# Performance work log

Measured on AMD Instinct MI355X. Metric: run time of the kernel, lower is better.

The kernel has to match this reference:

```python
import jax, jax.numpy as jnp
import numpy as np

D_IN = 200   # 4 * d_embeddings
H = 64       # hidden_size

def setup_inputs() -> dict:
    key = jax.random.key(0)
    ks = jax.random.split(key, 7)
    B, T = 4096, 128
    s_ih = 1.0 / np.sqrt(H)
    x = jax.random.normal(ks[0], (B, T, D_IN), dtype=jnp.float32)
    W_ih = jax.random.uniform(ks[1], (H, D_IN), minval=-s_ih, maxval=s_ih, dtype=jnp.float32)
    W_hh = jax.random.uniform(ks[2], (H, H), minval=-s_ih, maxval=s_ih, dtype=jnp.float32)
    b_ih = jax.random.uniform(ks[3], (H,), minval=-s_ih, maxval=s_ih, dtype=jnp.float32)
    b_hh = jax.random.uniform(ks[4], (H,), minval=-s_ih, maxval=s_ih, dtype=jnp.float32)
    W_out = jax.random.uniform(ks[5], (1, H), minval=-s_ih, maxval=s_ih, dtype=jnp.float32)
    b_out = jax.random.uniform(ks[6], (1,), minval=-s_ih, maxval=s_ih, dtype=jnp.float32)
    return {"x": x, "W_ih": W_ih, "W_hh": W_hh, "b_ih": b_ih, "b_hh": b_hh,
            "W_out": W_out, "b_out": b_out}

def reference(x, W_ih, W_hh, b_ih, b_hh, W_out, b_out):
    B = x.shape[0]
    # precompute input projection for all timesteps: [B, T, H]
    xp = jnp.einsum('btd,hd->bth', x, W_ih) + b_ih + b_hh
    def step(h, xt):
        h = jnp.tanh(xt + h @ W_hh.T)
        return h, None
    h0 = jnp.zeros((B, H), dtype=x.dtype)
    h_last, _ = jax.lax.scan(step, h0, jnp.swapaxes(xp, 0, 1))  # scan over time
    return jax.nn.sigmoid(h_last @ W_out.T + b_out)  # [B, 1]
```

## Files before the change

### kernel.cpp

```cpp
#include <hip/hip_runtime.h>
#include <hip/hip_bf16.h>


#define TSEQ 128
#define DIN  200
#define HID  64
#define TC   4
#define NCH  (TSEQ/TC)

typedef short bf16x8 __attribute__((ext_vector_type(8)));
typedef float f32x4  __attribute__((ext_vector_type(4)));

__device__ __forceinline__ short f2bf(float f) {
  __hip_bfloat16 h = __float2bfloat16(f);
  return __builtin_bit_cast(short, h);
}
__device__ __forceinline__ bf16x8 cvt8(f32x4 a, f32x4 b) {
  bf16x8 r;
#pragma unroll
  for (int i = 0; i < 4; ++i) { r[i] = f2bf(a[i]); r[4 + i] = f2bf(b[i]); }
  return r;
}
__device__ __forceinline__ float tanh_fast(float x) {
  float e = exp2f(x * 2.885390081777927f);
  float r = __builtin_amdgcn_rcpf(1.f + e);
  return __builtin_fmaf(-2.f, r, 1.f);
}

__global__ __launch_bounds__(256, 1) void rnn_fused(
    const float* __restrict__ x,   const float* __restrict__ Wih,
    const float* __restrict__ Whh, const float* __restrict__ bih,
    const float* __restrict__ bhh, const float* __restrict__ Wout,
    const float* __restrict__ bout, float* __restrict__ out)
{
  __shared__ float          xps[4][TC][HID][4];
  __shared__ unsigned short hb [4][4][HID];

  const int tid  = threadIdx.x;
  const int w    = tid >> 6;
  const int lane = tid & 63;
  const int m    = lane & 15;
  const int g    = lane >> 4;
  const int bw   = blockIdx.x * 16 + w * 4;

  const float* xrow = x + ((size_t)(bw + (m >> 2)) * TSEQ + (m & 3)) * DIN;

  f32x4 pA[7][2], pB[7][2];
  auto LOADC = [&](f32x4 (&P)[7][2], int c) {
    const float* p = xrow + (size_t)c * (TC * DIN);
#pragma unroll
    for (int ks = 0; ks < 7; ++ks) {
      const int d = ks * 32 + g * 8;
      if (d + 8 <= DIN) {
        P[ks][0] = *reinterpret_cast<const f32x4*>(p + d);
        P[ks][1] = *reinterpret_cast<const f32x4*>(p + d + 4);
      } else {
        P[ks][0] = (f32x4)0.f; P[ks][1] = (f32x4)0.f;
      }
    }
  };
  LOADC(pA, 0);
  LOADC(pB, 1);

  bf16x8 wihf[4][7];
#pragma unroll
  for (int nt = 0; nt < 4; ++nt) {
    const float* wr = Wih + (size_t)(nt * 16 + m) * DIN;
#pragma unroll
    for (int ks = 0; ks < 7; ++ks) {
      const int d = ks * 32 + g * 8;
      if (d + 8 <= DIN)
        wihf[nt][ks] = cvt8(*reinterpret_cast<const f32x4*>(wr + d),
                            *reinterpret_cast<const f32x4*>(wr + d + 4));
      else
        wihf[nt][ks] = (bf16x8)0;
    }
  }
  bf16x8 whhf[4][2];
#pragma unroll
  for (int nt = 0; nt < 4; ++nt)
#pragma unroll
    for (int hf = 0; hf < 2; ++hf) {
      const float* wr = Whh + (size_t)(nt * 16 + m) * HID + hf * 32 + g * 8;
      whhf[nt][hf] = cvt8(*reinterpret_cast<const f32x4*>(wr),
                          *reinterpret_cast<const f32x4*>(wr + 4));
    }
  float biasv[4];
#pragma unroll
  for (int nt = 0; nt < 4; ++nt) biasv[nt] = bih[nt * 16 + m] + bhh[nt * 16 + m];
  const float woutv = Wout[g * 16 + m];
  const float bout0 = bout[0];

  reinterpret_cast<unsigned int*>(&hb[w][0][0])[lane]      = 0u;
  reinterpret_cast<unsigned int*>(&hb[w][0][0])[lane + 64] = 0u;

  float vf[4];

  auto BODY = [&](f32x4 (&P)[7][2], int c) {
    bf16x8 afr[7];
#pragma unroll
    for (int ks = 0; ks < 7; ++ks) afr[ks] = cvt8(P[ks][0], P[ks][1]);
    if (c + 2 < NCH) LOADC(P, c + 2);

    f32x4 acc[4];
#pragma unroll
    for (int nt = 0; nt < 4; ++nt) acc[nt] = (f32x4)(biasv[nt]);
#pragma unroll
    for (int ks = 0; ks < 7; ++ks)
#pragma unroll
      for (int nt = 0; nt < 4; ++nt)
        acc[nt] = __builtin_amdgcn_mfma_f32_16x16x32_bf16(afr[ks], wihf[nt][ks], acc[nt], 0, 0, 0);

#pragma unroll
    for (int nt = 0; nt < 4; ++nt)
#pragma unroll
      for (int rr = 0; rr < 4; ++rr)
        xps[w][rr][nt * 16 + m][g] = acc[nt][rr];

#pragma unroll
    for (int tl = 0; tl < TC; ++tl) {
      f32x4 racc[4];
#pragma unroll
      for (int nt = 0; nt < 4; ++nt)
        racc[nt] = *reinterpret_cast<const f32x4*>(&xps[w][tl][nt * 16 + m][0]);
      bf16x8 ha0 = *reinterpret_cast<const bf16x8*>(&hb[w][m & 3][g * 8]);
      bf16x8 ha1 = *reinterpret_cast<const bf16x8*>(&hb[w][m & 3][32 + g * 8]);
#pragma unroll
      for (int nt = 0; nt < 4; ++nt) {
        racc[nt] = __builtin_amdgcn_mfma_f32_16x16x32_bf16(ha0, whhf[nt][0], racc[nt], 0, 0, 0);
        racc[nt] = __builtin_amdgcn_mfma_f32_16x16x32_bf16(ha1, whhf[nt][1], racc[nt], 0, 0, 0);
      }
#pragma unroll
      for (int r = 0; r < 4; ++r) {
        float v = (g == 0) ? racc[0][r] : (g == 1) ? racc[1][r]
                 : (g == 2) ? racc[2][r] : racc[3][r];
        v = tanh_fast(v);
        vf[r] = v;
        hb[w][r][g * 16 + m] = (unsigned short)f2bf(v);
      }
    }
  };

  for (int c = 0; c < NCH; c += 2) { BODY(pA, c); BODY(pB, c + 1); }

  f32x4 s;
#pragma unroll
  for (int r = 0; r < 4; ++r) s[r] = vf[r] * woutv;
#pragma unroll
  for (int mask = 1; mask < 64; mask <<= 1) {
#pragma unroll
    for (int r = 0; r < 4; ++r) s[r] += __shfl_xor(s[r], mask, 64);
  }
  if (lane == 0) {
    f32x4 o;
#pragma unroll
    for (int r = 0; r < 4; ++r) {
      const float z = s[r] + bout0;
      o[r] = __builtin_amdgcn_rcpf(1.f + exp2f(-z * 1.4426950408889634f));
    }
    *reinterpret_cast<f32x4*>(out + bw) = o;
  }
}

extern "C" void kernel_launch(void* const* d_in, const int* in_sizes, int n_in,
                              void* d_out, int out_size, void* d_ws, size_t ws_size,
                              hipStream_t stream) {
  const float* x    = (const float*)d_in[0];
  const float* Wih  = (const float*)d_in[1];
  const float* Whh  = (const float*)d_in[2];
  const float* bih  = (const float*)d_in[3];
  const float* bhh  = (const float*)d_in[4];
  const float* Wout = (const float*)d_in[5];
  const float* bout = (const float*)d_in[6];
  float* out = (float*)d_out;

  const int B = in_sizes[0] / (TSEQ * DIN);
  rnn_fused<<<dim3(B / 16), dim3(256), 0, stream>>>(x, Wih, Whh, bih, bhh, Wout, bout, out);
}
```

Before: 106.3 us.

## Split recurrence into two independent MFMA chains and software-pipeline the projection

The recurrent step now splits the 4 sequences per wave into two groups of 2 rows, each with its own MFMA accumulator chain (ra/rb), interleaved so the two dependency chains can hide each other's MFMA latency. The input projection for the next chunk is double-buffered in shared memory and issued ahead of the recurrent steps of the current chunk, with duplicated writes so each MFMA A-operand row holds the right sequence. This targets the serial latency of the recurrence. In exchange it uses more shared memory and duplicates stores, and only half of each MFMA's output rows carry useful work.

```diff
diff --git a/kernel.cpp b/kernel.cpp
--- a/kernel.cpp
+++ b/kernel.cpp
@@ -33,8 +33,8 @@
     const float* __restrict__ bhh, const float* __restrict__ Wout,
     const float* __restrict__ bout, float* __restrict__ out)
 {
-  __shared__ float          xps[4][TC][HID][4];
-  __shared__ unsigned short hb [4][4][HID];
+  __shared__ float          xps[2][4][2][TC][HID][4];
+  __shared__ unsigned short hb [4][2][2][HID];
 
   const int tid  = threadIdx.x;
   const int w    = tid >> 6;
@@ -47,10 +47,10 @@
 
   f32x4 pA[7][2], pB[7][2];
   auto LOADC = [&](f32x4 (&P)[7][2], int c) {
-    const float* p = xrow + (size_t)c * (TC * DIN);
 #pragma unroll
     for (int ks = 0; ks < 7; ++ks) {
       const int d = ks * 32 + g * 8;
+      const float* p = xrow + (size_t)c * (TC * DIN);
       if (d + 8 <= DIN) {
         P[ks][0] = *reinterpret_cast<const f32x4*>(p + d);
         P[ks][1] = *reinterpret_cast<const f32x4*>(p + d + 4);
@@ -59,8 +59,7 @@
       }
     }
   };
-  LOADC(pA, 0);
-  LOADC(pB, 1);
+  LOADC(pA, 0); LOADC(pB, 1);
 
   bf16x8 wihf[4][7];
 #pragma unroll
@@ -91,17 +90,13 @@
   const float woutv = Wout[g * 16 + m];
   const float bout0 = bout[0];
 
-  reinterpret_cast<unsigned int*>(&hb[w][0][0])[lane]      = 0u;
-  reinterpret_cast<unsigned int*>(&hb[w][0][0])[lane + 64] = 0u;
-
-  float vf[4];
-
-  auto BODY = [&](f32x4 (&P)[7][2], int c) {
+  reinterpret_cast<unsigned int*>(&hb[w][0][0][0])[lane]      = 0u;
+  reinterpret_cast<unsigned int*>(&hb[w][0][0][0])[lane + 64] = 0u;
+
+  auto PROJ = [&](f32x4 (&P)[7][2], float (*xq)[TC][HID][4]) {
     bf16x8 afr[7];
 #pragma unroll
     for (int ks = 0; ks < 7; ++ks) afr[ks] = cvt8(P[ks][0], P[ks][1]);
-    if (c + 2 < NCH) LOADC(P, c + 2);
-
     f32x4 acc[4];
 #pragma unroll
     for (int nt = 0; nt < 4; ++nt) acc[nt] = (f32x4)(biasv[nt]);
@@ -110,42 +105,69 @@
 #pragma unroll
       for (int nt = 0; nt < 4; ++nt)
         acc[nt] = __builtin_amdgcn_mfma_f32_16x16x32_bf16(afr[ks], wihf[nt][ks], acc[nt], 0, 0, 0);
-
 #pragma unroll
     for (int nt = 0; nt < 4; ++nt)
 #pragma unroll
-      for (int rr = 0; rr < 4; ++rr)
-        xps[w][rr][nt * 16 + m][g] = acc[nt][rr];
-
+      for (int rr = 0; rr < 4; ++rr) {
+        float v = acc[nt][rr];
+        float* bp = &xq[g >> 1][rr][nt * 16 + m][0];
+        bp[g & 1] = v; bp[(g & 1) + 2] = v;
+      }
+  };
+
+  float vf0 = 0.f, vf1 = 0.f, vf2 = 0.f, vf3 = 0.f;
+
+  auto STEPS = [&](float (*xq)[TC][HID][4]) {
 #pragma unroll
     for (int tl = 0; tl < TC; ++tl) {
-      f32x4 racc[4];
-#pragma unroll
-      for (int nt = 0; nt < 4; ++nt)
-        racc[nt] = *reinterpret_cast<const f32x4*>(&xps[w][tl][nt * 16 + m][0]);
-      bf16x8 ha0 = *reinterpret_cast<const bf16x8*>(&hb[w][m & 3][g * 8]);
-      bf16x8 ha1 = *reinterpret_cast<const bf16x8*>(&hb[w][m & 3][32 + g * 8]);
+      f32x4 ra[4], rb[4];
 #pragma unroll
       for (int nt = 0; nt < 4; ++nt) {
-        racc[nt] = __builtin_amdgcn_mfma_f32_16x16x32_bf16(ha0, whhf[nt][0], racc[nt], 0, 0, 0);
-        racc[nt] = __builtin_amdgcn_mfma_f32_16x16x32_bf16(ha1, whhf[nt][1], racc[nt], 0, 0, 0);
-      }
-#pragma unroll
-      for (int r = 0; r < 4; ++r) {
-        float v = (g == 0) ? racc[0][r] : (g == 1) ? racc[1][r]
-                 : (g == 2) ? racc[2][r] : racc[3][r];
-        v = tanh_fast(v);
-        vf[r] = v;
-        hb[w][r][g * 16 + m] = (unsigned short)f2bf(v);
-      }
+        ra[nt] = *reinterpret_cast<const f32x4*>(&xq[0][tl][nt * 16 + m][0]);
+        rb[nt] = *reinterpret_cast<const f32x4*>(&xq[1][tl][nt * 16 + m][0]);
+      }
+      bf16x8 aA0 = *reinterpret_cast<const bf16x8*>(&hb[w][0][m & 1][g * 8]);
+      bf16x8 aA1 = *reinterpret_cast<const bf16x8*>(&hb[w][0][m & 1][32 + g * 8]);
+      bf16x8 aB0 = *reinterpret_cast<const bf16x8*>(&hb[w][1][m & 1][g * 8]);
+      bf16x8 aB1 = *reinterpret_cast<const bf16x8*>(&hb[w][1][m & 1][32 + g * 8]);
+#pragma unroll
+      for (int nt = 0; nt < 4; ++nt) {
+        ra[nt] = __builtin_amdgcn_mfma_f32_16x16x32_bf16(aA0, whhf[nt][0], ra[nt], 0, 0, 0);
+        rb[nt] = __builtin_amdgcn_mfma_f32_16x16x32_bf16(aB0, whhf[nt][0], rb[nt], 0, 0, 0);
+      }
+#pragma unroll
+      for (int nt = 0; nt < 4; ++nt) {
+        ra[nt] = __builtin_amdgcn_mfma_f32_16x16x32_bf16(aA1, whhf[nt][1], ra[nt], 0, 0, 0);
+        rb[nt] = __builtin_amdgcn_mfma_f32_16x16x32_bf16(aB1, whhf[nt][1], rb[nt], 0, 0, 0);
+      }
+      float aLo = (g == 0) ? ra[0][0] : (g == 1) ? ra[1][0] : (g == 2) ? ra[2][0] : ra[3][0];
+      float aHi = (g == 0) ? ra[0][1] : (g == 1) ? ra[1][1] : (g == 2) ? ra[2][1] : ra[3][1];
+      float bLo = (g == 0) ? rb[0][0] : (g == 1) ? rb[1][0] : (g == 2) ? rb[2][0] : rb[3][0];
+      float bHi = (g == 0) ? rb[0][1] : (g == 1) ? rb[1][1] : (g == 2) ? rb[2][1] : rb[3][1];
+      aLo = tanh_fast(aLo); aHi = tanh_fast(aHi);
+      bLo = tanh_fast(bLo); bHi = tanh_fast(bHi);
+      const int col = g * 16 + m;
+      hb[w][0][0][col] = (unsigned short)f2bf(aLo);
+      hb[w][0][1][col] = (unsigned short)f2bf(aHi);
+      hb[w][1][0][col] = (unsigned short)f2bf(bLo);
+      hb[w][1][1][col] = (unsigned short)f2bf(bHi);
+      vf0 = aLo; vf1 = aHi; vf2 = bLo; vf3 = bHi;
     }
   };
 
-  for (int c = 0; c < NCH; c += 2) { BODY(pA, c); BODY(pB, c + 1); }
-
-  f32x4 s;
-#pragma unroll
-  for (int r = 0; r < 4; ++r) s[r] = vf[r] * woutv;
+  PROJ(pA, &xps[0][w][0]);
+  LOADC(pA, 2);
+
+  for (int c = 0; c < NCH; c += 2) {
+    PROJ(pB, &xps[1][w][0]);
+    if (c + 3 < NCH) LOADC(pB, c + 3);
+    STEPS(&xps[0][w][0]);
+    if (c + 2 < NCH) PROJ(pA, &xps[0][w][0]);
+    if (c + 4 < NCH) LOADC(pA, c + 4);
+    STEPS(&xps[1][w][0]);
+  }
+
+  f32x4 s; s[0] = vf0 * woutv; s[1] = vf1 * woutv; s[2] = vf2 * woutv; s[3] = vf3 * woutv;
 #pragma unroll
   for (int mask = 1; mask < 64; mask <<= 1) {
 #pragma unroll
```

New measurement: 111.8 us. +5.2%, slower.

## Halve rows per wave, stage x in LDS, share W_ih fragments via LDS

Applied to the files above, without the earlier changes.

Each wave now handles 2 batch rows instead of 4, and the grid doubles to B/8 blocks with launch bounds allowing 2 blocks per CU. The x input is loaded with coalesced contiguous f32x4 reads, converted to bf16 and staged through LDS in chunks of 8 timesteps. W_ih bf16 fragments move from registers into shared LDS to cut register pressure and allow more occupancy. The recurrence MFMA now wastes half its rows (rows duplicated), trading compute efficiency for more parallel waves that hide the serial dependency latency.

```diff
diff --git a/kernel.cpp b/kernel.cpp
--- a/kernel.cpp
+++ b/kernel.cpp
@@ -5,20 +5,26 @@
 #define TSEQ 128
 #define DIN  200
 #define HID  64
-#define TC   4
-#define NCH  (TSEQ/TC)
+#define CT   8
+#define NCH  (TSEQ/CT)
+#define STG_T 208
 
 typedef short bf16x8 __attribute__((ext_vector_type(8)));
 typedef float f32x4  __attribute__((ext_vector_type(4)));
+typedef float f32x2  __attribute__((ext_vector_type(2)));
+typedef unsigned int u32x2 __attribute__((ext_vector_type(2)));
 
-__device__ __forceinline__ short f2bf(float f) {
+__device__ __forceinline__ unsigned short f2bf(float f) {
   __hip_bfloat16 h = __float2bfloat16(f);
-  return __builtin_bit_cast(short, h);
+  return __builtin_bit_cast(unsigned short, h);
 }
 __device__ __forceinline__ bf16x8 cvt8(f32x4 a, f32x4 b) {
   bf16x8 r;
 #pragma unroll
-  for (int i = 0; i < 4; ++i) { r[i] = f2bf(a[i]); r[4 + i] = f2bf(b[i]); }
+  for (int i = 0; i < 4; ++i) {
+    r[i]     = (short)f2bf(a[i]);
+    r[4 + i] = (short)f2bf(b[i]);
+  }
   return r;
 }
 __device__ __forceinline__ float tanh_fast(float x) {
@@ -27,55 +33,49 @@
   return __builtin_fmaf(-2.f, r, 1.f);
 }
 
-__global__ __launch_bounds__(256, 1) void rnn_fused(
+__global__ __launch_bounds__(256, 2) void rnn_fused(
     const float* __restrict__ x,   const float* __restrict__ Wih,
     const float* __restrict__ Whh, const float* __restrict__ bih,
     const float* __restrict__ bhh, const float* __restrict__ Wout,
     const float* __restrict__ bout, float* __restrict__ out)
 {
-  __shared__ float          xps[4][TC][HID][4];
-  __shared__ unsigned short hb [4][4][HID];
+  __shared__ unsigned short wihL[28][64][8];
+  __shared__ unsigned short stg[4][2][CT * STG_T];
+  __shared__ float          xpl[4][CT][HID][2];
+  __shared__ unsigned short hbl[4][2][72];
 
   const int tid  = threadIdx.x;
   const int w    = tid >> 6;
   const int lane = tid & 63;
   const int m    = lane & 15;
   const int g    = lane >> 4;
-  const int bw   = blockIdx.x * 16 + w * 4;
+  const int r0   = blockIdx.x * 8 + w * 2;
 
-  const float* xrow = x + ((size_t)(bw + (m >> 2)) * TSEQ + (m & 3)) * DIN;
-
-  f32x4 pA[7][2], pB[7][2];
-  auto LOADC = [&](f32x4 (&P)[7][2], int c) {
-    const float* p = xrow + (size_t)c * (TC * DIN);
+  f32x4 pld[2][7];
+  auto LOADC = [&](int c) {
 #pragma unroll
-    for (int ks = 0; ks < 7; ++ks) {
-      const int d = ks * 32 + g * 8;
-      if (d + 8 <= DIN) {
-        P[ks][0] = *reinterpret_cast<const f32x4*>(p + d);
-        P[ks][1] = *reinterpret_cast<const f32x4*>(p + d + 4);
-      } else {
-        P[ks][0] = (f32x4)0.f; P[ks][1] = (f32x4)0.f;
+    for (int r = 0; r < 2; ++r) {
+      const float* bp = x + (size_t)(r0 + r) * (TSEQ * DIN) + (size_t)c * (CT * DIN);
+#pragma unroll
+      for (int i = 0; i < 7; ++i) {
+        if (i < 6)          pld[r][i] = *reinterpret_cast<const f32x4*>(bp + i * 256 + lane * 4);
+        else if (lane < 16) pld[r][6] = *reinterpret_cast<const f32x4*>(bp + 1536 + lane * 4);
       }
     }
   };
-  LOADC(pA, 0);
-  LOADC(pB, 1);
+  LOADC(0);
 
-  bf16x8 wihf[4][7];
-#pragma unroll
-  for (int nt = 0; nt < 4; ++nt) {
-    const float* wr = Wih + (size_t)(nt * 16 + m) * DIN;
-#pragma unroll
-    for (int ks = 0; ks < 7; ++ks) {
-      const int d = ks * 32 + g * 8;
-      if (d + 8 <= DIN)
-        wihf[nt][ks] = cvt8(*reinterpret_cast<const f32x4*>(wr + d),
-                            *reinterpret_cast<const f32x4*>(wr + d + 4));
-      else
-        wihf[nt][ks] = (bf16x8)0;
+  for (int f = w; f < 28; f += 4) {
+    const int nt = f / 7, ks = f % 7;
+    const int d  = ks * 32 + g * 8;
+    bf16x8 v = (bf16x8)0;
+    if (d + 8 <= DIN) {
+      const float* wr = Wih + (size_t)(nt * 16 + m) * DIN + d;
+      v = cvt8(*reinterpret_cast<const f32x4*>(wr), *reinterpret_cast<const f32x4*>(wr + 4));
     }
+    *reinterpret_cast<bf16x8*>(&wihL[f][lane][0]) = v;
   }
+
   bf16x8 whhf[4][2];
 #pragma unroll
   for (int nt = 0; nt < 4; ++nt)
@@ -88,77 +88,93 @@
   float biasv[4];
 #pragma unroll
   for (int nt = 0; nt < 4; ++nt) biasv[nt] = bih[nt * 16 + m] + bhh[nt * 16 + m];
-  const float woutv = Wout[g * 16 + m];
+  const float woutl = Wout[lane];
   const float bout0 = bout[0];
 
-  reinterpret_cast<unsigned int*>(&hb[w][0][0])[lane]      = 0u;
-  reinterpret_cast<unsigned int*>(&hb[w][0][0])[lane + 64] = 0u;
+  {
+    unsigned int* hz = reinterpret_cast<unsigned int*>(&hbl[w][0][0]);
+    hz[lane] = 0u;
+    if (lane < 8) hz[64 + lane] = 0u;
+  }
+  __syncthreads();
 
-  float vf[4];
+  float hv0 = 0.f, hv1 = 0.f;
 
-  auto BODY = [&](f32x4 (&P)[7][2], int c) {
-    bf16x8 afr[7];
+  for (int c = 0; c < NCH; ++c) {
 #pragma unroll
-    for (int ks = 0; ks < 7; ++ks) afr[ks] = cvt8(P[ks][0], P[ks][1]);
-    if (c + 2 < NCH) LOADC(P, c + 2);
+    for (int i = 0; i < 7; ++i) {
+      if (i < 6 || lane < 16) {
+        const int fi  = i * 256 + lane * 4;
+        const int tl_ = fi / 200;
+        const int c2  = fi - tl_ * 200;
+#pragma unroll
+        for (int r = 0; r < 2; ++r) {
+          f32x4 p = pld[r][i];
+          u32x2 d2;
+          d2[0] = (unsigned)f2bf(p[0]) | ((unsigned)f2bf(p[1]) << 16);
+          d2[1] = (unsigned)f2bf(p[2]) | ((unsigned)f2bf(p[3]) << 16);
+          *reinterpret_cast<u32x2*>(&stg[w][r][tl_ * STG_T + c2]) = d2;
+        }
+      }
+    }
+    if (c + 1 < NCH) LOADC(c + 1);
 
     f32x4 acc[4];
 #pragma unroll
     for (int nt = 0; nt < 4; ++nt) acc[nt] = (f32x4)(biasv[nt]);
+    {
+      const unsigned short* sp = &stg[w][m >> 3][(m & 7) * STG_T];
 #pragma unroll
-    for (int ks = 0; ks < 7; ++ks)
+      for (int ks = 0; ks < 7; ++ks) {
+        bf16x8 av = *reinterpret_cast<const bf16x8*>(sp + (ks < 6 ? ks * 32 + g * 8 : 192));
+        if (ks == 6 && g != 0) av = (bf16x8)0;
 #pragma unroll
-      for (int nt = 0; nt < 4; ++nt)
-        acc[nt] = __builtin_amdgcn_mfma_f32_16x16x32_bf16(afr[ks], wihf[nt][ks], acc[nt], 0, 0, 0);
-
+        for (int nt = 0; nt < 4; ++nt) {
+          bf16x8 bv = *reinterpret_cast<const bf16x8*>(&wihL[nt * 7 + ks][lane][0]);
+          acc[nt] = __builtin_amdgcn_mfma_f32_16x16x32_bf16(av, bv, acc[nt], 0, 0, 0);
+        }
+      }
+    }
 #pragma unroll
     for (int nt = 0; nt < 4; ++nt)
 #pragma unroll
       for (int rr = 0; rr < 4; ++rr)
-        xps[w][rr][nt * 16 + m][g] = acc[nt][rr];
+        xpl[w][(g & 1) * 4 + rr][nt * 16 + m][g >> 1] = acc[nt][rr];
 
 #pragma unroll
-    for (int tl = 0; tl < TC; ++tl) {
+    for (int tl = 0; tl < CT; ++tl) {
       f32x4 racc[4];
 #pragma unroll
+      for (int nt = 0; nt < 4; ++nt) {
+        f32x2 q = *reinterpret_cast<const f32x2*>(&xpl[w][tl][nt * 16 + m][0]);
+        racc[nt][0] = q[0]; racc[nt][1] = q[1]; racc[nt][2] = q[0]; racc[nt][3] = q[1];
+      }
+      bf16x8 ha0 = *reinterpret_cast<const bf16x8*>(&hbl[w][m & 1][g * 8]);
+      bf16x8 ha1 = *reinterpret_cast<const bf16x8*>(&hbl[w][m & 1][32 + g * 8]);
+#pragma unroll
       for (int nt = 0; nt < 4; ++nt)
-        racc[nt] = *reinterpret_cast<const f32x4*>(&xps[w][tl][nt * 16 + m][0]);
-      bf16x8 ha0 = *reinterpret_cast<const bf16x8*>(&hb[w][m & 3][g * 8]);
-      bf16x8 ha1 = *reinterpret_cast<const bf16x8*>(&hb[w][m & 3][32 + g * 8]);
+        racc[nt] = __builtin_amdgcn_mfma_f32_16x16x32_bf16(ha0, whhf[nt][0], racc[nt], 0, 0, 0);
 #pragma unroll
-      for (int nt = 0; nt < 4; ++nt) {
-        racc[nt] = __builtin_amdgcn_mfma_f32_16x16x32_bf16(ha0, whhf[nt][0], racc[nt], 0, 0, 0);
+      for (int nt = 0; nt < 4; ++nt)
         racc[nt] = __builtin_amdgcn_mfma_f32_16x16x32_bf16(ha1, whhf[nt][1], racc[nt], 0, 0, 0);
-      }
-#pragma unroll
-      for (int r = 0; r < 4; ++r) {
-        float v = (g == 0) ? racc[0][r] : (g == 1) ? racc[1][r]
-                 : (g == 2) ? racc[2][r] : racc[3][r];
-        v = tanh_fast(v);
-        vf[r] = v;
-        hb[w][r][g * 16 + m] = (unsigned short)f2bf(v);
-      }
+      float v0 = (g == 0) ? racc[0][0] : (g == 1) ? racc[1][0] : (g == 2) ? racc[2][0] : racc[3][0];
+      float v1 = (g == 0) ? racc[0][1] : (g == 1) ? racc[1][1] : (g == 2) ? racc[2][1] : racc[3][1];
+      v0 = tanh_fast(v0); v1 = tanh_fast(v1);
+      hv0 = v0; hv1 = v1;
+      hbl[w][0][lane] = f2bf(v0);
+      hbl[w][1][lane] = f2bf(v1);
     }
-  };
+  }
 
-  for (int c = 0; c < NCH; c += 2) { BODY(pA, c); BODY(pB, c + 1); }
-
-  f32x4 s;
-#pragma unroll
-  for (int r = 0; r < 4; ++r) s[r] = vf[r] * woutv;
+  float s0 = hv0 * woutl, s1 = hv1 * woutl;
 #pragma unroll
   for (int mask = 1; mask < 64; mask <<= 1) {
-#pragma unroll
-    for (int r = 0; r < 4; ++r) s[r] += __shfl_xor(s[r], mask, 64);
+    s0 += __shfl_xor(s0, mask, 64);
+    s1 += __shfl_xor(s1, mask, 64);
   }
   if (lane == 0) {
-    f32x4 o;
-#pragma unroll
-    for (int r = 0; r < 4; ++r) {
-      const float z = s[r] + bout0;
-      o[r] = __builtin_amdgcn_rcpf(1.f + exp2f(-z * 1.4426950408889634f));
-    }
-    *reinterpret_cast<f32x4*>(out + bw) = o;
+    out[r0]     = __builtin_amdgcn_rcpf(1.f + exp2f(-(s0 + bout0) * 1.4426950408889634f));
+    out[r0 + 1] = __builtin_amdgcn_rcpf(1.f + exp2f(-(s1 + bout0) * 1.4426950408889634f));
   }
 }
 
@@ -175,5 +191,5 @@
   float* out = (float*)d_out;
 
   const int B = in_sizes[0] / (TSEQ * DIN);
-  rnn_fused<<<dim3(B / 16), dim3(256), 0, stream>>>(x, Wih, Whh, bih, bhh, Wout, bout, out);
+  rnn_fused<<<dim3(B / 8), dim3(256), 0, stream>>>(x, Wih, Whh, bih, bhh, Wout, bout, out);
 }
```

New measurement: 107.2 us. No clear change (+0.9%).
